# Performance work log

Measured on AMD Instinct MI355X. Metric: run time of the kernel, lower is better.

## Reference

```python
import jax, jax.numpy as jnp
import numpy as np

T, B, H, NH = 1024, 4, 1024, 16
D = H // NH


def setup_inputs() -> dict:
    key = jax.random.key(0)
    ks = jax.random.split(key, 8)
    s = 0.02
    return {
        "x": jax.random.normal(ks[0], (T, B, H), jnp.float32),
        "pos": jax.random.normal(ks[1], (2 * T - 1, 1, H), jnp.float32),
        "attn_mask": jnp.zeros((T, T), jnp.bool_),
        "ln_w": jnp.ones((H,), jnp.float32),
        "ln_b": jnp.zeros((H,), jnp.float32),
        "in_proj_w": jax.random.normal(ks[2], (3 * H, H), jnp.float32) * s,
        "in_proj_b": jnp.zeros((3 * H,), jnp.float32),
        "pos_proj_w": jax.random.normal(ks[3], (H, H), jnp.float32) * s,
        "r_w_bias": jax.random.normal(ks[4], (NH, D), jnp.float32) * s,
        "r_r_bias": jax.random.normal(ks[5], (NH, D), jnp.float32) * s,
        "out_proj_w": jax.random.normal(ks[6], (H, H), jnp.float32) * s,
        "out_proj_b": jnp.zeros((H,), jnp.float32),
    }


def _layer_norm(x, w, b, eps=1e-5):
    m = jnp.mean(x, axis=-1, keepdims=True)
    v = jnp.var(x, axis=-1, keepdims=True)
    return (x - m) * jax.lax.rsqrt(v + eps) * w + b


def _rel_shift(x):
    # x: [qlen, 2*qlen-1, B, NH] -> Transformer-XL relative shift
    q = x.shape[0]
    zero_pad = jnp.zeros((q, 1) + x.shape[2:], x.dtype)
    xp = jnp.concatenate([zero_pad, x], axis=1)            # [q, 2q, B, NH]
    xp = xp.reshape((x.shape[1] + 1, q) + x.shape[2:])     # [2q, q, B, NH]
    return xp[1:].reshape(x.shape)                         # [q, 2q-1, B, NH]


def reference(x, pos, attn_mask, ln_w, ln_b, in_proj_w, in_proj_b,
              pos_proj_w, r_w_bias, r_r_bias, out_proj_w, out_proj_b):
    # pre-norm
    qn = _layer_norm(x, ln_w, ln_b)                        # [T,B,H]
    # fused qkv projection
    qkv = qn @ in_proj_w.T + in_proj_b                     # [T,B,3H]
    q, k, v = jnp.split(qkv, 3, axis=-1)
    q = q.reshape(T, B, NH, D)
    k = k.reshape(T, B, NH, D)
    v = v.reshape(T, B, NH, D)
    # relative position keys (bias-free projection)
    r = (pos[:, 0] @ pos_proj_w.T).reshape(2 * T - 1, NH, D)
    # content term (AC) and position term (BD), Transformer-XL style
    AC = jnp.einsum('ibnd,jbnd->ijbn', q + r_w_bias, k)    # [T,T,B,NH]
    BD = jnp.einsum('ibnd,jnd->ijbn', q + r_r_bias, r)     # [T,2T-1,B,NH]
    BD = _rel_shift(BD)[:, :T]                             # [T,T,B,NH]
    scale = 1.0 / np.sqrt(D).astype(np.float32)
    score = (AC + BD) * scale
    score = jnp.where(attn_mask[:, :, None, None], -jnp.inf, score)
    p = jax.nn.softmax(score, axis=1)                      # coverage
    out = jnp.einsum('ijbn,jbnd->ibnd', p, v).reshape(T, B, H)
    o = out @ out_proj_w.T + out_proj_b                    # residual dropout = identity (eval)
    return o
```

## Files before the change

### kernel.cpp

```cpp
#include <hip/hip_runtime.h>
#include <hip/hip_bf16.h>
#include <math.h>

#define T_DIM 1024
#define B_DIM 4
#define H_DIM 1024
#define NHEAD 16
#define DHEAD 64
#define NROWS (T_DIM * B_DIM)
#define LPOS  (2 * T_DIM - 1)
#define QS    (3 * H_DIM)

typedef __attribute__((ext_vector_type(8))) short bfrag;
typedef __attribute__((ext_vector_type(4))) short sh4;
typedef __attribute__((ext_vector_type(4))) float facc;

static __device__ __forceinline__ short f2bf(float f) {
    return __builtin_bit_cast(short, __float2bfloat16(f));
}
static __device__ __forceinline__ float bf2f(short s) {
    unsigned u = ((unsigned)(unsigned short)s) << 16;
    return __builtin_bit_cast(float, u);
}

#define GLD16(g, l) __builtin_amdgcn_global_load_lds( \
    (const __attribute__((address_space(1))) void*)(g), \
    (__attribute__((address_space(3))) void*)(l), 16, 0, 0)

__global__ __launch_bounds__(256) void prep_kernel(
    const float* __restrict__ x, const float* __restrict__ lnw,
    const float* __restrict__ lnb, short* __restrict__ qn,
    const float* __restrict__ s0, short* __restrict__ d0, int c0,
    const float* __restrict__ s1, short* __restrict__ d1, int c1,
    const float* __restrict__ s2, short* __restrict__ d2, int c2,
    const float* __restrict__ s3, short* __restrict__ d3, int c3) {
    __shared__ float red0[4], red1[4];
    const int bid = blockIdx.x;
    const int tid = threadIdx.x;
    if (bid < NROWS) {
        const float* xr = x + (size_t)bid * H_DIM;
        short* yr = qn + (size_t)bid * H_DIM;
        float4 v = reinterpret_cast<const float4*>(xr)[tid];
        float s  = v.x + v.y + v.z + v.w;
        float sq = v.x * v.x + v.y * v.y + v.z * v.z + v.w * v.w;
        #pragma unroll
        for (int m = 32; m; m >>= 1) {
            s  += __shfl_xor(s, m);
            sq += __shfl_xor(sq, m);
        }
        int wave = tid >> 6, lane = tid & 63;
        if (lane == 0) { red0[wave] = s; red1[wave] = sq; }
        __syncthreads();
        float tot   = red0[0] + red0[1] + red0[2] + red0[3];
        float totsq = red1[0] + red1[1] + red1[2] + red1[3];
        float mean = tot * (1.0f / H_DIM);
        float var  = totsq * (1.0f / H_DIM) - mean * mean;
        float rstd = rsqrtf(var + 1e-5f);
        float4 wv = reinterpret_cast<const float4*>(lnw)[tid];
        float4 bv = reinterpret_cast<const float4*>(lnb)[tid];
        sh4 o;
        o[0] = f2bf((v.x - mean) * rstd * wv.x + bv.x);
        o[1] = f2bf((v.y - mean) * rstd * wv.y + bv.y);
        o[2] = f2bf((v.z - mean) * rstd * wv.z + bv.z);
        o[3] = f2bf((v.w - mean) * rstd * wv.w + bv.w);
        reinterpret_cast<sh4*>(yr)[tid] = o;
    } else {
        int i = (bid - NROWS) * 256 + tid;
        const float* s; short* d; int off;
        if      (i < c0)                { s = s0; d = d0; off = i; }
        else if (i < c0 + c1)           { s = s1; d = d1; off = i - c0; }
        else if (i < c0 + c1 + c2)      { s = s2; d = d2; off = i - c0 - c1; }
        else if (i < c0 + c1 + c2 + c3) { s = s3; d = d3; off = i - c0 - c1 - c2; }
        else return;
        const float* sp = s + (size_t)off * 8;
        float4 a = *(const float4*)(sp);
        float4 b = *(const float4*)(sp + 4);
        bfrag f;
        f[0] = f2bf(a.x); f[1] = f2bf(a.y); f[2] = f2bf(a.z); f[3] = f2bf(a.w);
        f[4] = f2bf(b.x); f[5] = f2bf(b.y); f[6] = f2bf(b.z); f[7] = f2bf(b.w);
        *(bfrag*)(d + (size_t)off * 8) = f;
    }
}

template<int MODE>
static __device__ __forceinline__ void gemm_body(
    const short* __restrict__ A, const short* __restrict__ B,
    const float* __restrict__ bias, void* __restrict__ Cv,
    int M, int N, int K, int gx, int nblk, int bid,
    short (*As)[64], short (*Bs)[64]) {
    const int tid = threadIdx.x;
    const int w4 = tid >> 6, l = tid & 63;
    const int lc = l & 15, lg = l >> 4;
    const int wr = w4 >> 1, wc = w4 & 1;

    const int cpx = nblk >> 3;
    const int nl = (bid & 7) * cpx + (bid >> 3);
    const int row0 = (nl / gx) * 128, col0 = (nl % gx) * 128;

    const int srow = l >> 3;
    const int schunk = ((l & 7) ^ srow) * 8;
    const int Mm1 = M - 1;

    facc acc[4][4];
    #pragma unroll
    for (int i = 0; i < 4; ++i)
        #pragma unroll
        for (int j = 0; j < 4; ++j) acc[i][j] = (facc){0.f, 0.f, 0.f, 0.f};

    for (int k0 = 0; k0 < K; k0 += 64) {
        #pragma unroll
        for (int p = 0; p < 4; ++p) {
            int rA = p * 32 + w4 * 8 + srow;
            int ga = row0 + rA; if (ga > Mm1) ga = Mm1;
            GLD16(A + (size_t)ga * K + k0 + schunk,
                  (char*)As + p * 4096 + w4 * 1024);
            GLD16(B + (size_t)(col0 + rA) * K + k0 + schunk,
                  (char*)Bs + p * 4096 + w4 * 1024);
        }
        __syncthreads();

        bfrag af[4][2], bfr[4][2];
        #pragma unroll
        for (int fr = 0; fr < 4; ++fr) {
            const int ra = wr * 64 + fr * 16 + lc;
            #pragma unroll
            for (int ks = 0; ks < 2; ++ks)
                af[fr][ks] = *(const bfrag*)&As[ra][(((ks * 4 + lg) ^ (ra & 7)) << 3)];
        }
        #pragma unroll
        for (int fc = 0; fc < 4; ++fc) {
            const int rb = wc * 64 + fc * 16 + lc;
            #pragma unroll
            for (int ks = 0; ks < 2; ++ks)
                bfr[fc][ks] = *(const bfrag*)&Bs[rb][(((ks * 4 + lg) ^ (rb & 7)) << 3)];
        }
        #pragma unroll
        for (int fr = 0; fr < 4; ++fr)
            #pragma unroll
            for (int fc = 0; fc < 4; ++fc)
                #pragma unroll
                for (int ks = 0; ks < 2; ++ks)
                    acc[fr][fc] = __builtin_amdgcn_mfma_f32_16x16x32_bf16(
                        af[fr][ks], bfr[fc][ks], acc[fr][fc], 0, 0, 0);
        __syncthreads();
    }

    #pragma unroll
    for (int fc = 0; fc < 4; ++fc) {
        const int gc = col0 + wc * 64 + fc * 16 + lc;
        const float bv = bias ? bias[gc] : 0.f;
        #pragma unroll
        for (int fr = 0; fr < 4; ++fr) {
            #pragma unroll
            for (int rg = 0; rg < 4; ++rg) {
                const int gr = row0 + wr * 64 + fr * 16 + lg * 4 + rg;
                if (gr < M) {
                    float o = acc[fr][fc][rg] + bv;
                    if constexpr (MODE == 0) ((float*)Cv)[(size_t)gr * N + gc] = o;
                    else                     ((short*)Cv)[(size_t)gr * N + gc] = f2bf(o);
                }
            }
        }
    }
}

__global__ __launch_bounds__(256) void gemm_dual(
    const short* __restrict__ A0, const short* __restrict__ B0,
    const float* __restrict__ bias0, short* __restrict__ C0,
    const short* __restrict__ A1, const short* __restrict__ B1,
    short* __restrict__ C1) {
    __shared__ short As[128][64];
    __shared__ short Bs[128][64];
    const int bid = blockIdx.x;
    if (bid < 768)
        gemm_body<1>(A0, B0, bias0, C0, NROWS, QS, H_DIM, QS / 128, 768, bid, As, Bs);
    else
        gemm_body<1>(A1, B1, nullptr, C1, LPOS, H_DIM, H_DIM, H_DIM / 128, 128, bid - 768, As, Bs);
}

__global__ __launch_bounds__(256) void gemm_f32out(
    const short* __restrict__ A, const short* __restrict__ B,
    const float* __restrict__ bias, float* __restrict__ C) {
    __shared__ short As[128][64];
    __shared__ short Bs[128][64];
    gemm_body<0>(A, B, bias, C, NROWS, H_DIM, H_DIM, H_DIM / 128, 256, blockIdx.x, As, Bs);
}

__global__ __launch_bounds__(256) void vtrans_kernel(const short* __restrict__ qkv,
                                                     short* __restrict__ vT) {
    __shared__ short T[64][72];
    const int tt = blockIdx.x, hh = blockIdx.y, b = blockIdx.z;
    const int tid = threadIdx.x;
    const int w = tid >> 6, lane = tid & 63;

    const int tg = tt * 64 + lane;
    const short* src = qkv + (size_t)(tg * B_DIM + b) * QS + 2 * H_DIM + hh * 64 + w * 16;
    bfrag v0 = *(const bfrag*)(src);
    bfrag v1 = *(const bfrag*)(src + 8);
    #pragma unroll
    for (int e = 0; e < 8; ++e) T[w * 16 + e][lane] = v0[e];
    #pragma unroll
    for (int e = 0; e < 8; ++e) T[w * 16 + 8 + e][lane] = v1[e];
    __syncthreads();

    const int hd = tid >> 2, tc = tid & 3;
    bfrag o0 = *(const bfrag*)&T[hd][tc * 16];
    bfrag o1 = *(const bfrag*)&T[hd][tc * 16 + 8];
    short* dst = vT + (((size_t)(b * H_DIM + hh * 64 + hd)) << 10) + tt * 64 + tc * 16;
    *(bfrag*)(dst) = o0;
    *(bfrag*)(dst + 8) = o1;
}

__global__ __launch_bounds__(256) void attn_mfma(const short* __restrict__ qkv,
                                                 const short* __restrict__ r,
                                                 const short* __restrict__ vt,
                                                 const float* __restrict__ rwb,
                                                 const float* __restrict__ rrb,
                                                 short* __restrict__ out) {
    __shared__ short Ks[64][64];
    __shared__ short Vt[64][64];
    __shared__ short Rs[128][64];
    __shared__ short BDs[4][16][84];
    __shared__ short Ps[4][16][76];

    const int d_   = blockIdx.y * 16 + blockIdx.x;
    const int slot = d_ >> 3, xcd = d_ & 7;
    const int bn   = xcd + 8 * (slot >> 4);
    const int i0   = (slot & 15) * 64;
    const int b    = bn >> 4;
    const int n    = bn & 15;

    const int tid = threadIdx.x;
    const int w   = tid >> 6;
    const int l   = tid & 63;
    const int lg  = l >> 4;
    const int lc  = l & 15;
    const int hoff = n * DHEAD;

    const int srow8 = l >> 3;
    const int sc8   = ((l & 7) ^ srow8) * 8;

    bfrag qw[2], qr[2];
    {
        const int row = i0 + 16 * w + lc;
        const short* qrow = qkv + (size_t)(row * B_DIM + b) * QS + hoff;
        #pragma unroll
        for (int ks = 0; ks < 2; ++ks) {
            const int d0 = ks * 32 + lg * 8;
            bfrag qv = *(const bfrag*)(qrow + d0);
            float4 wa = *(const float4*)(rwb + hoff + d0);
            float4 wb = *(const float4*)(rwb + hoff + d0 + 4);
            float4 ra = *(const float4*)(rrb + hoff + d0);
            float4 rb = *(const float4*)(rrb + hoff + d0 + 4);
            const float sc = 0.125f * 1.44269504f;
            float wf[8] = {wa.x, wa.y, wa.z, wa.w, wb.x, wb.y, wb.z, wb.w};
            float rf[8] = {ra.x, ra.y, ra.z, ra.w, rb.x, rb.y, rb.z, rb.w};
            bfrag fw, fr;
            #pragma unroll
            for (int e = 0; e < 8; ++e) {
                float qf = bf2f(qv[e]);
                fw[e] = f2bf((qf + wf[e]) * sc);
                fr[e] = f2bf((qf + rf[e]) * sc);
            }
            qw[ks] = fw; qr[ks] = fr;
        }
    }

    facc ofr[4];
    #pragma unroll
    for (int d = 0; d < 4; ++d) ofr[d] = (facc){0.f, 0.f, 0.f, 0.f};
    float lrow[4] = {0.f, 0.f, 0.f, 0.f};
    const int wbase = 16 * (3 - w);

    const short* kp0 = qkv + ((size_t)((w * 2 + 0) * 8 + srow8) * B_DIM + b) * QS + H_DIM + hoff + sc8;
    const short* kp1 = qkv + ((size_t)((w * 2 + 1) * 8 + srow8) * B_DIM + b) * QS + H_DIM + hoff + sc8;
    const short* vp0 = vt + (((size_t)(b * H_DIM + hoff + (w * 2 + 0) * 8 + srow8)) << 10) + sc8;
    const short* vp1 = vt + (((size_t)(b * H_DIM + hoff + (w * 2 + 1) * 8 + srow8)) << 10) + sc8;
    const size_t kstep = (size_t)64 * B_DIM * QS;
    bfrag* const ksd0 = (bfrag*)((char*)Ks + (w * 2 + 0) * 1024 + l * 16);
    bfrag* const ksd1 = (bfrag*)((char*)Ks + (w * 2 + 1) * 1024 + l * 16);
    bfrag* const vtd0 = (bfrag*)((char*)Vt + (w * 2 + 0) * 1024 + l * 16);
    bfrag* const vtd1 = (bfrag*)((char*)Vt + (w * 2 + 1) * 1024 + l * 16);

    bfrag stK0, stK1, stV0, stV1, stR[4];

    auto load_regs = [&](int jt) {
        const int l_min = jt * 64 + 960 - i0;
        stK0 = *(const bfrag*)(kp0 + (size_t)jt * kstep);
        stK1 = *(const bfrag*)(kp1 + (size_t)jt * kstep);
        stV0 = *(const bfrag*)(vp0 + jt * 64);
        stV1 = *(const bfrag*)(vp1 + jt * 64);
        #pragma unroll
        for (int p = 0; p < 4; ++p) {
            const int c16 = w * 4 + p;
            int lrw = l_min + c16 * 8 + srow8; if (lrw > 2046) lrw = 2046;
            stR[p] = *(const bfrag*)(r + (size_t)lrw * H_DIM + hoff + sc8);
        }
    };
    auto write_lds = [&]() {
        *ksd0 = stK0; *ksd1 = stK1;
        *vtd0 = stV0; *vtd1 = stV1;
        #pragma unroll
        for (int p = 0; p < 4; ++p)
            *(bfrag*)((char*)Rs + (w * 4 + p) * 1024 + l * 16) = stR[p];
    };

    load_regs(0);
    write_lds();
    __syncthreads();

    for (int jt = 0; jt < 16; ++jt) {
        if (jt < 15) load_regs(jt + 1);

        __builtin_amdgcn_s_setprio(1);
        facc sfr[4];
        #pragma unroll
        for (int js = 0; js < 4; ++js) {
            sfr[js] = (facc){-4.f, -4.f, -4.f, -4.f};
            const int jrow = js * 16 + lc;
            #pragma unroll
            for (int ks = 0; ks < 2; ++ks) {
                const int ch = (ks * 4 + lg) ^ (jrow & 7);
                bfrag bf = *(const bfrag*)&Ks[jrow][ch << 3];
                sfr[js] = __builtin_amdgcn_mfma_f32_16x16x32_bf16(qw[ks], bf, sfr[js], 0, 0, 0);
            }
        }
        #pragma unroll
        for (int ls = 0; ls < 5; ++ls) {
            facc bd = (facc){-4.f, -4.f, -4.f, -4.f};
            const int rrow = wbase + ls * 16 + lc;
            #pragma unroll
            for (int ks = 0; ks < 2; ++ks) {
                const int ch = (ks * 4 + lg) ^ (rrow & 7);
                bfrag bf = *(const bfrag*)&Rs[rrow][ch << 3];
                bd = __builtin_amdgcn_mfma_f32_16x16x32_bf16(qr[ks], bf, bd, 0, 0, 0);
            }
            #pragma unroll
            for (int rg = 0; rg < 4; ++rg)
                BDs[w][lg * 4 + rg][ls * 16 + lc] = f2bf(bd[rg]);
        }
        __builtin_amdgcn_s_setprio(0);

        #pragma unroll
        for (int js = 0; js < 4; ++js)
            #pragma unroll
            for (int rg = 0; rg < 4; ++rg) {
                const int irow = lg * 4 + rg;
                float v = sfr[js][rg] + bf2f(BDs[w][irow][js * 16 + lc - irow + 15]);
                float p = exp2f(v);
                lrow[rg] += p;
                Ps[w][irow][js * 16 + lc] = f2bf(p);
            }

        bfrag pf[2];
        #pragma unroll
        for (int ks = 0; ks < 2; ++ks)
            pf[ks] = *(const bfrag*)&Ps[w][lc][ks * 32 + lg * 8];
        __builtin_amdgcn_s_setprio(1);
        #pragma unroll
        for (int d = 0; d < 4; ++d) {
            #pragma unroll
            for (int ks = 0; ks < 2; ++ks) {
                const int vr = d * 16 + lc;
                const int ch = (ks * 4 + lg) ^ (vr & 7);
                bfrag vf = *(const bfrag*)&Vt[vr][ch << 3];
                ofr[d] = __builtin_amdgcn_mfma_f32_16x16x32_bf16(pf[ks], vf, ofr[d], 0, 0, 0);
            }
        }
        __builtin_amdgcn_s_setprio(0);

        __syncthreads();
        if (jt < 15) {
            write_lds();
            __syncthreads();
        }
    }

    #pragma unroll
    for (int m = 1; m < 16; m <<= 1)
        #pragma unroll
        for (int rg = 0; rg < 4; ++rg)
            lrow[rg] += __shfl_xor(lrow[rg], m);

    #pragma unroll
    for (int rg = 0; rg < 4; ++rg) {
        const float inv = 1.0f / lrow[rg];
        const int row = i0 + 16 * w + lg * 4 + rg;
        short* orow = out + (size_t)(row * B_DIM + b) * H_DIM + hoff;
        #pragma unroll
        for (int d = 0; d < 4; ++d)
            orow[d * 16 + lc] = f2bf(ofr[d][rg] * inv);
    }
}

extern "C" void kernel_launch(void* const* d_in, const int* in_sizes, int n_in,
                              void* d_out, int out_size, void* d_ws, size_t ws_size,
                              hipStream_t stream) {
    const float* x          = (const float*)d_in[0];
    const float* pos        = (const float*)d_in[1];
    const float* ln_w       = (const float*)d_in[3];
    const float* ln_b       = (const float*)d_in[4];
    const float* in_proj_w  = (const float*)d_in[5];
    const float* in_proj_b  = (const float*)d_in[6];
    const float* pos_proj_w = (const float*)d_in[7];
    const float* r_w_bias   = (const float*)d_in[8];
    const float* r_r_bias   = (const float*)d_in[9];
    const float* out_proj_w = (const float*)d_in[10];
    const float* out_proj_b = (const float*)d_in[11];
    float* out = (float*)d_out;

    short* qn   = (short*)d_ws;
    short* qkv  = qn + (size_t)NROWS * H_DIM;
    short* rbuf = qkv + (size_t)NROWS * QS;
    short* wi   = rbuf + (size_t)2048 * H_DIM;
    short* wp   = wi + (size_t)QS * H_DIM;
    short* wo   = wp + (size_t)H_DIM * H_DIM;
    short* posb = wo + (size_t)H_DIM * H_DIM;
    short* vT   = posb + (size_t)2048 * H_DIM;

    const int c0 = (LPOS * H_DIM) / 8;
    const int c1 = (QS * H_DIM) / 8;
    const int c2 = (H_DIM * H_DIM) / 8;
    const int c3 = c2;
    const int nchunk = c0 + c1 + c2 + c3;
    const int cvtblk = (nchunk + 255) / 256;
    prep_kernel<<<NROWS + cvtblk, 256, 0, stream>>>(
        x, ln_w, ln_b, qn,
        pos, posb, c0, in_proj_w, wi, c1, pos_proj_w, wp, c2, out_proj_w, wo, c3);

    gemm_dual<<<768 + 128, 256, 0, stream>>>(qn, wi, in_proj_b, qkv, posb, wp, rbuf);

    vtrans_kernel<<<dim3(16, 16, 4), 256, 0, stream>>>(qkv, vT);

    attn_mfma<<<dim3(T_DIM / 64, B_DIM * NHEAD), 256, 0, stream>>>(
        qkv, rbuf, vT, r_w_bias, r_r_bias, qn);

    gemm_f32out<<<256, 256, 0, stream>>>(qn, wo, out_proj_b, out);
}
```

Before: 175.5 us.

## Double attention block to 8 waves covering 128 query rows sharing K/V/R tiles

The attention kernel now launches 512-thread blocks of 8 waves, each block covering 128 query rows instead of 64. Every wave loads one K row group and one V row group plus three R row groups, so each staged K/V tile is reused by twice as many query rows, and the R window grows to 192 rows. The BD and P scratch buffers are merged into one LDS array to keep shared memory small, and the grid is flattened to 512 blocks with a remapped XCD-aware index. The trade-off is fewer, larger blocks with higher register and LDS pressure per block, which may lower occupancy or leave the GPU less evenly loaded.

```diff
diff --git a/kernel.cpp b/kernel.cpp
--- a/kernel.cpp
+++ b/kernel.cpp
@@ -211,22 +211,21 @@
     *(bfrag*)(dst + 8) = o1;
 }
 
-__global__ __launch_bounds__(256) void attn_mfma(const short* __restrict__ qkv,
-                                                 const short* __restrict__ r,
-                                                 const short* __restrict__ vt,
-                                                 const float* __restrict__ rwb,
-                                                 const float* __restrict__ rrb,
-                                                 short* __restrict__ out) {
+__global__ __launch_bounds__(512, 4) void attn_mfma(const short* __restrict__ qkv,
+                                                    const short* __restrict__ r,
+                                                    const short* __restrict__ vt,
+                                                    const float* __restrict__ rwb,
+                                                    const float* __restrict__ rrb,
+                                                    short* __restrict__ out) {
     __shared__ short Ks[64][64];
     __shared__ short Vt[64][64];
-    __shared__ short Rs[128][64];
-    __shared__ short BDs[4][16][84];
-    __shared__ short Ps[4][16][76];
-
-    const int d_   = blockIdx.y * 16 + blockIdx.x;
+    __shared__ short Rs[192][64];
+    __shared__ short BDPs[8][16][84];
+
+    const int d_   = blockIdx.x;
     const int slot = d_ >> 3, xcd = d_ & 7;
-    const int bn   = xcd + 8 * (slot >> 4);
-    const int i0   = (slot & 15) * 64;
+    const int bn   = xcd + 8 * (slot >> 3);
+    const int i0   = (slot & 7) * 128;
     const int b    = bn >> 4;
     const int n    = bn & 15;
 
@@ -270,39 +269,33 @@
     #pragma unroll
     for (int d = 0; d < 4; ++d) ofr[d] = (facc){0.f, 0.f, 0.f, 0.f};
     float lrow[4] = {0.f, 0.f, 0.f, 0.f};
-    const int wbase = 16 * (3 - w);
-
-    const short* kp0 = qkv + ((size_t)((w * 2 + 0) * 8 + srow8) * B_DIM + b) * QS + H_DIM + hoff + sc8;
-    const short* kp1 = qkv + ((size_t)((w * 2 + 1) * 8 + srow8) * B_DIM + b) * QS + H_DIM + hoff + sc8;
-    const short* vp0 = vt + (((size_t)(b * H_DIM + hoff + (w * 2 + 0) * 8 + srow8)) << 10) + sc8;
-    const short* vp1 = vt + (((size_t)(b * H_DIM + hoff + (w * 2 + 1) * 8 + srow8)) << 10) + sc8;
+    const int wbase = 16 * (7 - w);
+
+    const short* kp = qkv + ((size_t)(w * 8 + srow8) * B_DIM + b) * QS + H_DIM + hoff + sc8;
+    const short* vp = vt + (((size_t)(b * H_DIM + hoff + w * 8 + srow8)) << 10) + sc8;
     const size_t kstep = (size_t)64 * B_DIM * QS;
-    bfrag* const ksd0 = (bfrag*)((char*)Ks + (w * 2 + 0) * 1024 + l * 16);
-    bfrag* const ksd1 = (bfrag*)((char*)Ks + (w * 2 + 1) * 1024 + l * 16);
-    bfrag* const vtd0 = (bfrag*)((char*)Vt + (w * 2 + 0) * 1024 + l * 16);
-    bfrag* const vtd1 = (bfrag*)((char*)Vt + (w * 2 + 1) * 1024 + l * 16);
-
-    bfrag stK0, stK1, stV0, stV1, stR[4];
+    bfrag* const ksd = (bfrag*)((char*)Ks + w * 1024 + l * 16);
+    bfrag* const vtd = (bfrag*)((char*)Vt + w * 1024 + l * 16);
+
+    bfrag stK, stV, stR[3];
 
     auto load_regs = [&](int jt) {
-        const int l_min = jt * 64 + 960 - i0;
-        stK0 = *(const bfrag*)(kp0 + (size_t)jt * kstep);
-        stK1 = *(const bfrag*)(kp1 + (size_t)jt * kstep);
-        stV0 = *(const bfrag*)(vp0 + jt * 64);
-        stV1 = *(const bfrag*)(vp1 + jt * 64);
-        #pragma unroll
-        for (int p = 0; p < 4; ++p) {
-            const int c16 = w * 4 + p;
-            int lrw = l_min + c16 * 8 + srow8; if (lrw > 2046) lrw = 2046;
+        const int l_min = jt * 64 + 896 - i0;
+        stK = *(const bfrag*)(kp + (size_t)jt * kstep);
+        stV = *(const bfrag*)(vp + jt * 64);
+        #pragma unroll
+        for (int p = 0; p < 3; ++p) {
+            const int rr = (w * 3 + p) * 8 + srow8;
+            int lrw = l_min + rr; if (lrw > 2046) lrw = 2046;
             stR[p] = *(const bfrag*)(r + (size_t)lrw * H_DIM + hoff + sc8);
         }
     };
     auto write_lds = [&]() {
-        *ksd0 = stK0; *ksd1 = stK1;
-        *vtd0 = stV0; *vtd1 = stV1;
-        #pragma unroll
-        for (int p = 0; p < 4; ++p)
-            *(bfrag*)((char*)Rs + (w * 4 + p) * 1024 + l * 16) = stR[p];
+        *ksd = stK;
+        *vtd = stV;
+        #pragma unroll
+        for (int p = 0; p < 3; ++p)
+            *(bfrag*)((char*)Rs + (w * 3 + p) * 1024 + l * 16) = stR[p];
     };
 
     load_regs(0);
@@ -337,7 +330,7 @@
             }
             #pragma unroll
             for (int rg = 0; rg < 4; ++rg)
-                BDs[w][lg * 4 + rg][ls * 16 + lc] = f2bf(bd[rg]);
+                BDPs[w][lg * 4 + rg][ls * 16 + lc] = f2bf(bd[rg]);
         }
         __builtin_amdgcn_s_setprio(0);
 
@@ -346,16 +339,16 @@
             #pragma unroll
             for (int rg = 0; rg < 4; ++rg) {
                 const int irow = lg * 4 + rg;
-                float v = sfr[js][rg] + bf2f(BDs[w][irow][js * 16 + lc - irow + 15]);
+                float v = sfr[js][rg] + bf2f(BDPs[w][irow][js * 16 + lc - irow + 15]);
                 float p = exp2f(v);
                 lrow[rg] += p;
-                Ps[w][irow][js * 16 + lc] = f2bf(p);
+                BDPs[w][irow][js * 16 + lc] = f2bf(p);
             }
 
         bfrag pf[2];
         #pragma unroll
         for (int ks = 0; ks < 2; ++ks)
-            pf[ks] = *(const bfrag*)&Ps[w][lc][ks * 32 + lg * 8];
+            pf[ks] = *(const bfrag*)&BDPs[w][lc][ks * 32 + lg * 8];
         __builtin_amdgcn_s_setprio(1);
         #pragma unroll
         for (int d = 0; d < 4; ++d) {
@@ -432,7 +425,7 @@
 
     vtrans_kernel<<<dim3(16, 16, 4), 256, 0, stream>>>(qkv, vT);
 
-    attn_mfma<<<dim3(T_DIM / 64, B_DIM * NHEAD), 256, 0, stream>>>(
+    attn_mfma<<<512, 512, 0, stream>>>(
         qkv, rbuf, vT, r_w_bias, r_r_bias, qn);
 
     gemm_f32out<<<256, 256, 0, stream>>>(qn, wo, out_proj_b, out);
```

New measurement: 165.1 us. -5.9%, faster.
